# Kernel optimization log

Hardware: AMD Instinct MI355X
Metric: run time of the kernel (lower is better)

## Reference

```python
import jax, jax.numpy as jnp
import numpy as np

C = 64        # channel_n
HID = 128     # hidden_size
HEADS = 4
HD = 16       # head_dim = embed_dim // heads, embed_dim overwritten to channel_n
INNER = HEADS * HD  # 64
MLP = 64
H = W = 64    # img_size
B = 8
STEPS = 6
IN_CH = 1     # input_channels
SCALE = HD ** -0.5


def conv3x3_reflect(x, w, b):
    # x: [B,C,H,W], w: [O,I,3,3] -- reflect padding like nn.Conv2d(padding_mode='reflect')
    xp = jnp.pad(x, ((0, 0), (0, 0), (1, 1), (1, 1)), mode='reflect')
    y = jax.lax.conv_general_dilated(xp, w, (1, 1), 'VALID',
                                     dimension_numbers=('NCHW', 'OIHW', 'NCHW'))
    return y + b[None, :, None, None]


def layernorm(x, w, b, axes):
    mu = jnp.mean(x, axis=axes, keepdims=True)
    var = jnp.var(x, axis=axes, keepdims=True)
    return (x - mu) * jax.lax.rsqrt(var + 1e-5) * w + b


def localize(t, h, w):
    # t: [B,heads,n,d] -> [B,heads,n,9,d]; zero-padded 3x3 neighbourhoods
    # (equivalent to grouped conv with 9 unit-impulse filters, padding='same')
    b, nh, n, d = t.shape
    g = t.reshape(b, nh, h, w, d)
    gp = jnp.pad(g, ((0, 0), (0, 0), (1, 1), (1, 1), (0, 0)))
    nb = jnp.stack([gp[:, :, i:i + h, j:j + w, :]
                    for i in range(3) for j in range(3)], axis=4)
    return nb.reshape(b, nh, n, 9, d)


def attn_block(t, ln_w, ln_b, qkv_w, out_w, out_b):
    y = layernorm(t, ln_w, ln_b, -1)
    qkv = y @ qkv_w.T                              # [B,n,3*inner]
    q, k, v = jnp.split(qkv, 3, axis=-1)
    to_heads = lambda z: z.reshape(z.shape[0], z.shape[1], HEADS, HD).transpose(0, 2, 1, 3)
    q, k, v = to_heads(q), to_heads(k), to_heads(v)   # [B,h,n,d]
    kl = localize(k, H, W)                          # [B,h,n,9,d]
    vl = localize(v, H, W)
    dots = jnp.einsum('bhnd,bhnkd->bhnk', q, kl) * SCALE
    a = jax.nn.softmax(dots, axis=-1)               # [B,h,n,9]
    o = jnp.einsum('bhnk,bhnkd->bhnd', a, vl)
    o = o.transpose(0, 2, 1, 3).reshape(t.shape[0], t.shape[1], INNER)
    return o @ out_w.T + out_b


def ff_block(t, ln_w, ln_b, w1, b1, w2, b2):
    y = layernorm(t, ln_w, ln_b, -1)
    y = jax.nn.gelu(y @ w1.T + b1, approximate=False)
    return y @ w2.T + b2


def setup_inputs() -> dict:
    key = jax.random.key(0)
    ks = jax.random.split(key, 20)
    s = 0.02
    inp = {
        'x': jax.random.normal(ks[0], (B, H, W, C), jnp.float32),
        'masks': jax.random.bernoulli(ks[1], 0.5, (STEPS, B, H, W, 1)),
        'p0_w': jax.random.normal(ks[2], (C, C, 3, 3)) * s,
        'p0_b': jnp.zeros((C,)),
        'p1_w': jax.random.normal(ks[3], (C, C, 3, 3)) * s,
        'p1_b': jnp.zeros((C,)),
        'fc0_w': jax.random.normal(ks[4], (HID, 3 * C)) * s,
        'fc0_b': jnp.zeros((HID,)),
        'fc1_w': jax.random.normal(ks[5], (C, HID)) * s,  # zero-init in torch; random here for a non-trivial test
        'norm0_w': jnp.ones((H, W, HID)),
        'norm0_b': jnp.zeros((H, W, HID)),
        'ln1_w': jnp.ones((C,)),
        'ln1_b': jnp.zeros((C,)),
        'qkv_w': jax.random.normal(ks[6], (3 * INNER, C)) * s,
        'out_w': jax.random.normal(ks[7], (C, INNER)) * s,
        'out_b': jnp.zeros((C,)),
        'ln2_w': jnp.ones((C,)),
        'ln2_b': jnp.zeros((C,)),
        'ff1_w': jax.random.normal(ks[8], (MLP, C)) * s,
        'ff1_b': jnp.zeros((MLP,)),
        'ff2_w': jax.random.normal(ks[9], (C, MLP)) * s,
        'ff2_b': jnp.zeros((C,)),
        'steps': STEPS,
    }
    return inp


def reference(x, masks, p0_w, p0_b, p1_w, p1_b, fc0_w, fc0_b, fc1_w,
              norm0_w, norm0_b, ln1_w, ln1_b, qkv_w, out_w, out_b,
              ln2_w, ln2_b, ff1_w, ff1_b, ff2_w, ff2_b, steps):
    def step(xc, mask):
        # ---- NCA perception + update (BackboneNCA.perceive + fc0/relu/norm/fc1) ----
        xt = xc.transpose(0, 3, 1, 2)                      # [B,C,H,W]
        y1 = conv3x3_reflect(xt, p0_w, p0_b)
        y2 = conv3x3_reflect(xt, p1_w, p1_b)
        p = jnp.concatenate([xt, y1, y2], 1).transpose(0, 2, 3, 1)  # [B,H,W,3C]
        hd = jax.nn.relu(p @ fc0_w.T + fc0_b)              # [B,H,W,HID]
        hd = layernorm(hd, norm0_w, norm0_b, (-3, -2, -1))  # norm0 over [H,W,HID]
        dx = hd @ fc1_w.T                                   # [B,H,W,C]
        dx = dx * mask.astype(xc.dtype)                     # stochastic fire
        xn = xc + dx
        # ---- ViT block with localized (3x3 windowed) attention ----
        t = xn.reshape(B, H * W, C)
        t = t + attn_block(t, ln1_w, ln1_b, qkv_w, out_w, out_b)
        t = t + ff_block(t, ln2_w, ln2_b, ff1_w, ff1_b, ff2_w, ff2_b)
        xn = t.reshape(B, H, W, C)
        # keep input channels unchanged
        xn = jnp.concatenate([xc[..., :IN_CH], xn[..., IN_CH:]], axis=-1)
        return xn, None

    out, _ = jax.lax.scan(step, x, masks)
    return out
```

## Files before the change

### kernel.cpp

```cpp
#include <hip/hip_runtime.h>
#include <hip/hip_bf16.h>

typedef __hip_bfloat16 bf16;
typedef __attribute__((ext_vector_type(8))) short bf16x8;
typedef __attribute__((ext_vector_type(4))) float f32x4;

#define NSTEP 6

static __device__ __forceinline__ float b2f(bf16 v) { return __bfloat162float(v); }

static __device__ __forceinline__ float ldp(const void* p, int i, int md) {
    return md ? ((const float*)p)[i] : b2f(((const bf16*)p)[i]);
}
static __device__ __forceinline__ float finz(float v) {
    return (v == v && v * 0.0f == 0.0f) ? v : 0.0f;
}
static __device__ __forceinline__ unsigned short f2bfu(float v) {
    bf16 h = __float2bfloat16(v);
    return *(unsigned short*)&h;
}

static __device__ __forceinline__ void ld_bf8(const bf16* p, float* f) {
    union { uint4 u; unsigned short s[8]; } r;
    r.u = *(const uint4*)p;
#pragma unroll
    for (int j = 0; j < 8; ++j) f[j] = __uint_as_float(((unsigned)r.s[j]) << 16);
}
static __device__ __forceinline__ void ldp8(const void* p, int i, int md, float* f) {
    if (md) {
        const float* fp = (const float*)p + i;
        float4 a = *(const float4*)fp, b = *(const float4*)(fp + 4);
        f[0]=a.x; f[1]=a.y; f[2]=a.z; f[3]=a.w; f[4]=b.x; f[5]=b.y; f[6]=b.z; f[7]=b.w;
    } else {
        ld_bf8((const bf16*)p + i, f);
    }
}
static __device__ __forceinline__ uint4 pk_bf8(const float* f) {
    union { uint4 u; unsigned short s[8]; } r;
#pragma unroll
    for (int j = 0; j < 8; ++j) r.s[j] = f2bfu(f[j]);
    return r.u;
}


__global__ void k_detect(const uint4* __restrict__ m4,
                         const uint4* __restrict__ x4,
                         int* __restrict__ flags, float* __restrict__ accv) {
    __shared__ int s3f, sup, slo, sf32;
    int t = threadIdx.x;
    if (t == 0) { s3f = 0; sup = 0; slo = 0; sf32 = 0; }
    if (t < 96) accv[t] = 0.f;
    __syncthreads();
    int l3f = 0, lup = 0, llo = 0, lf = 0;
    for (int i = t; i < 3072; i += 256) {
        uint4 v = m4[i];
        const unsigned* d = (const unsigned*)&v;
#pragma unroll
        for (int j = 0; j < 4; ++j) {
            unsigned w = d[j];
            unsigned x3f = w ^ 0x3F3F3F3Fu;
            if ((x3f - 0x01010101u) & ~x3f & 0x80808080u) l3f = 1;
            if (w & 0xFFFFFF00u) lup = 1;
            if (w & 0x0000FFFFu) llo = 1;
        }
    }
    for (int i = t; i < 4096; i += 256) {
        uint4 v = x4[i];
        const unsigned* d = (const unsigned*)&v;
#pragma unroll
        for (int j = 0; j < 4; ++j) {
            unsigned bb = (d[j] >> 8) & 0x7Fu;
            if (bb > 0x48u) lf = 1;
        }
    }
    if (l3f) atomicOr(&s3f, 1);
    if (lup) atomicOr(&sup, 1);
    if (llo) atomicOr(&slo, 1);
    if (lf)  atomicOr(&sf32, 1);
    __syncthreads();
    if (t == 0) {
        int mode;
        if (!s3f && !sup) mode = 0;
        else if (!s3f)    mode = 1;
        else if (slo)     mode = 2;
        else              mode = 3;
        flags[0] = mode;
        flags[1] = sf32;
    }
}


template <int MD>
static __device__ __forceinline__ void cast_body(
    const void* __restrict__ x, float* __restrict__ xout, int i) {
    float f[8];
    ldp8(x, i * 8, MD, f);
#pragma unroll
    for (int j = 0; j < 8; ++j) f[j] = finz(f[j]);
    *(float4*)&xout[i * 8]     = make_float4(f[0], f[1], f[2], f[3]);
    *(float4*)&xout[i * 8 + 4] = make_float4(f[4], f[5], f[6], f[7]);
}

template <int MD>
static __device__ __forceinline__ void cwfold_body(
    const void* __restrict__ p0w, const void* __restrict__ p1w,
    const void* __restrict__ p0b, const void* __restrict__ p1b,
    const void* __restrict__ fc0w, const void* __restrict__ fc0b,
    short* __restrict__ cw, float* __restrict__ hbias,
    float* __restrict__ sfc0, int o, int t) {
    if (t < 192) sfc0[t] = ldp(fc0w, o * 192 + t, MD);
    __syncthreads();
    int u0 = t, u1 = t + 256, u2 = t + 512;
    bool has2 = (u2 < 576);
    float a0 = (u0 % 9 == 4) ? sfc0[u0 / 9] : 0.f;
    float a1 = (u1 % 9 == 4) ? sfc0[u1 / 9] : 0.f;
    float a2 = (has2 && u2 % 9 == 4) ? sfc0[u2 / 9] : 0.f;
#pragma unroll 8
    for (int c = 0; c < 64; ++c) {
        float f0 = sfc0[64 + c];
        float f1 = sfc0[128 + c];
        int base = c * 576;
        a0 = fmaf(ldp(p0w, base + u0, MD), f0, a0);
        a0 = fmaf(ldp(p1w, base + u0, MD), f1, a0);
        a1 = fmaf(ldp(p0w, base + u1, MD), f0, a1);
        a1 = fmaf(ldp(p1w, base + u1, MD), f1, a1);
        if (has2) {
            a2 = fmaf(ldp(p0w, base + u2, MD), f0, a2);
            a2 = fmaf(ldp(p1w, base + u2, MD), f1, a2);
        }
    }
    cw[o * 576 + (u0 % 9) * 64 + u0 / 9] = (short)f2bfu(a0);
    cw[o * 576 + (u1 % 9) * 64 + u1 / 9] = (short)f2bfu(a1);
    if (has2) cw[o * 576 + (u2 % 9) * 64 + u2 / 9] = (short)f2bfu(a2);
    if (t < 64) {
        int c = t;
        float s = ldp(p0b, c, MD) * sfc0[64 + c]
                + ldp(p1b, c, MD) * sfc0[128 + c];
#pragma unroll
        for (int off = 32; off > 0; off >>= 1) s += __shfl_down(s, off, 64);
        if (c == 0) hbias[o] = ldp(fc0b, o, MD) + s;
    }
}

template <int MD>
static __device__ __forceinline__ void lnfold_body(
    const void* __restrict__ fc1w, const void* __restrict__ n0w,
    const void* __restrict__ n0b, float* __restrict__ wsum,
    float* __restrict__ bconst, int pos, int c) {
    float ws = 0.f, bs = 0.f;
#pragma unroll 8
    for (int j8 = 0; j8 < 128; j8 += 8) {
        float wv[8], bv[8], fv[8];
        ldp8(n0w, pos * 128 + j8, MD, wv);
        ldp8(n0b, pos * 128 + j8, MD, bv);
        ldp8(fc1w, c * 128 + j8, MD, fv);
#pragma unroll
        for (int jj = 0; jj < 8; ++jj) {
            float f = __uint_as_float(((unsigned)f2bfu(fv[jj])) << 16);
            ws = fmaf(wv[jj], f, ws);
            bs = fmaf(bv[jj], f, bs);
        }
    }
    wsum[pos * 64 + c]   = ws;
    bconst[pos * 64 + c] = bs;
}

__global__ void k_prep_w(const void* __restrict__ p0w, const void* __restrict__ p1w,
                         const void* __restrict__ p0b, const void* __restrict__ p1b,
                         const void* __restrict__ fc0w, const void* __restrict__ fc0b,
                         const void* __restrict__ fc1w, const void* __restrict__ qkvw,
                         const void* __restrict__ outw, const void* __restrict__ ff1w,
                         const void* __restrict__ ff2w,
                         short* __restrict__ cw, short* __restrict__ packs,
                         float* __restrict__ hbias,
                         const void* __restrict__ n0w, const void* __restrict__ n0b,
                         float* __restrict__ wsum, float* __restrict__ bconst,
                         const int* __restrict__ mflags) {
    __shared__ float sfc0[192];
    int md = mflags[1];
    int t = threadIdx.x;
    int bk = blockIdx.x;
    if (bk < 128) {
        int j = bk * 256 + t;
        float v;
        if      (j < 8192)  v = ldp(fc1w, j, md);
        else if (j < 20480) v = ldp(qkvw, j - 8192, md);
        else if (j < 24576) v = ldp(outw, j - 20480, md);
        else if (j < 28672) v = ldp(ff1w, j - 24576, md);
        else                v = ldp(ff2w, j - 28672, md);
        packs[j] = (short)f2bfu(v);
    } else if (bk < 256) {
        int o = bk - 128;
        if (md) cwfold_body<1>(p0w, p1w, p0b, p1b, fc0w, fc0b, cw, hbias, sfc0, o, t);
        else    cwfold_body<0>(p0w, p1w, p0b, p1b, fc0w, fc0b, cw, hbias, sfc0, o, t);
    } else {
        int fbk = bk - 256;
        int c = t & 63, pl = t >> 6;
        int pos = fbk * 4 + pl;
        if (md) lnfold_body<1>(fc1w, n0w, n0b, wsum, bconst, pos, c);
        else    lnfold_body<0>(fc1w, n0w, n0b, wsum, bconst, pos, c);
    }
}

__global__ void k_prep_cast(const void* __restrict__ x, float* __restrict__ xout,
                            const int* __restrict__ mflags) {
    int md = mflags[1];
    int i = blockIdx.x * 256 + threadIdx.x;
    if (md) cast_body<1>(x, xout, i);
    else    cast_body<0>(x, xout, i);
}


__global__ __launch_bounds__(512) void k_perceive(
    const float* __restrict__ xin, const short* __restrict__ cw,
    const short* __restrict__ fc1s, const float* __restrict__ hbias,
    const void* __restrict__ n0w, const int* __restrict__ mflags,
    float* __restrict__ t1, float* __restrict__ accv, int step)
{
    __shared__ __align__(16) short xpad_s[3 * 66 * 72];
    __shared__ __align__(16) short hd_s[64 * 136];
    __shared__ float red[32];
    int md = mflags[1];
    int bh = blockIdx.x;
    int b = bh >> 6, h = bh & 63;
    int t = threadIdx.x;

    for (int e = t; e < 1536; e += 512) {
        int c8 = e & 7, w = (e >> 3) & 63, r = e >> 9;
        int hr = h - 1 + r; hr = hr < 0 ? -hr : (hr > 63 ? 126 - hr : hr);
        const float* src = xin + ((((b << 6) + hr) << 6) | w) * 64 + c8 * 8;
        float f[8];
        float4 v0 = *(const float4*)src, v1 = *(const float4*)(src + 4);
        f[0]=v0.x; f[1]=v0.y; f[2]=v0.z; f[3]=v0.w; f[4]=v1.x; f[5]=v1.y; f[6]=v1.z; f[7]=v1.w;
        *(uint4*)&xpad_s[((r * 66) + w + 1) * 72 + c8 * 8] = pk_bf8(f);
    }
    if (t < 48) {
        int c8 = t & 7, side = (t >> 3) & 1, r = t >> 4;
        int hr = h - 1 + r; hr = hr < 0 ? -hr : (hr > 63 ? 126 - hr : hr);
        int wsrc = side ? 62 : 1, wp = side ? 65 : 0;
        const float* src = xin + ((((b << 6) + hr) << 6) | wsrc) * 64 + c8 * 8;
        float f[8];
        float4 v0 = *(const float4*)src, v1 = *(const float4*)(src + 4);
        f[0]=v0.x; f[1]=v0.y; f[2]=v0.z; f[3]=v0.w; f[4]=v1.x; f[5]=v1.y; f[6]=v1.z; f[7]=v1.w;
        *(uint4*)&xpad_s[((r * 66) + wp) * 72 + c8 * 8] = pk_bf8(f);
    }
    __syncthreads();

    int og  = __builtin_amdgcn_readfirstlane(t >> 6);
    int l   = t & 63, nl = l & 15, q = l >> 4;
    int mt0 = (og & 1) * 2;
    int nt0 = (og >> 1) * 2;
    int o0  = nt0 * 16 + nl, o1 = o0 + 16;

    f32x4 acc[2][2];
#pragma unroll
    for (int i = 0; i < 2; ++i)
#pragma unroll
        for (int j = 0; j < 2; ++j) acc[i][j] = (f32x4){0.f, 0.f, 0.f, 0.f};

    for (int kt = 0; kt < 18; ++kt) {
        int kk = kt >> 1, c0 = (kt & 1) << 5;
        int r = kk / 3, cxi = kk - r * 3;
        bf16x8 b0 = *(const bf16x8*)(cw + o0 * 576 + kt * 32 + q * 8);
        bf16x8 b1 = *(const bf16x8*)(cw + o1 * 576 + kt * 32 + q * 8);
        bf16x8 a0 = *(const bf16x8*)&xpad_s[((r * 66) + mt0 * 16 + nl + cxi) * 72 + c0 + q * 8];
        bf16x8 a1 = *(const bf16x8*)&xpad_s[((r * 66) + mt0 * 16 + 16 + nl + cxi) * 72 + c0 + q * 8];
        acc[0][0] = __builtin_amdgcn_mfma_f32_16x16x32_bf16(a0, b0, acc[0][0], 0, 0, 0);
        acc[0][1] = __builtin_amdgcn_mfma_f32_16x16x32_bf16(a0, b1, acc[0][1], 0, 0, 0);
        acc[1][0] = __builtin_amdgcn_mfma_f32_16x16x32_bf16(a1, b0, acc[1][0], 0, 0, 0);
        acc[1][1] = __builtin_amdgcn_mfma_f32_16x16x32_bf16(a1, b1, acc[1][1], 0, 0, 0);
    }

    float lsum = 0.f, lsq = 0.f;
    {
        float hb0 = hbias[o0], hb1 = hbias[o1];
#pragma unroll
        for (int i = 0; i < 2; ++i)
#pragma unroll
            for (int j = 0; j < 2; ++j) {
                int oo = j ? o1 : o0;
                float bb = j ? hb1 : hb0;
#pragma unroll
                for (int r2 = 0; r2 < 4; ++r2) {
                    int m = (mt0 + i) * 16 + q * 4 + r2;
                    float v = fmaxf(acc[i][j][r2] + bb, 0.f);
                    unsigned short hu = f2bfu(v);
                    hd_s[m * 136 + oo] = (short)hu;
                    float vr = __uint_as_float(((unsigned)hu) << 16);
                    lsum += vr; lsq += vr * vr;
                }
            }
    }
#pragma unroll
    for (int off = 32; off > 0; off >>= 1) {
        lsum += __shfl_down(lsum, off, 64);
        lsq  += __shfl_down(lsq,  off, 64);
    }
    if (l == 0) { red[og] = lsum; red[16 + og] = lsq; }
    __syncthreads();
    if (t == 0) {
        float a = 0.f, s2 = 0.f;
#pragma unroll
        for (int w = 0; w < 8; ++w) { a += red[w]; s2 += red[16 + w]; }
        atomicAdd(&accv[step * 16 + b * 2],     a);
        atomicAdd(&accv[step * 16 + b * 2 + 1], s2);
    }

    for (int e = t; e < 1024; e += 512) {
        int pos = e >> 4, j8 = (e & 15) * 8;
        float hv[8], wv[8];
        ld_bf8((const bf16*)&hd_s[pos * 136 + j8], hv);
        ldp8(n0w, (h * 64 + pos) * 128 + j8, md, wv);
#pragma unroll
        for (int j = 0; j < 8; ++j) hv[j] *= wv[j];
        *(uint4*)&hd_s[pos * 136 + j8] = pk_bf8(hv);
    }
    __syncthreads();

    {
        int mt = og & 3, nh = og >> 2;
        int to0 = nh * 32 + nl, to1 = to0 + 16;
        f32x4 a0 = (f32x4){0.f,0.f,0.f,0.f}, a1 = (f32x4){0.f,0.f,0.f,0.f};
#pragma unroll
        for (int kt = 0; kt < 4; ++kt) {
            bf16x8 av = *(const bf16x8*)&hd_s[(mt * 16 + nl) * 136 + kt * 32 + q * 8];
            bf16x8 b0 = *(const bf16x8*)(fc1s + to0 * 128 + kt * 32 + q * 8);
            bf16x8 b1 = *(const bf16x8*)(fc1s + to1 * 128 + kt * 32 + q * 8);
            a0 = __builtin_amdgcn_mfma_f32_16x16x32_bf16(av, b0, a0, 0, 0, 0);
            a1 = __builtin_amdgcn_mfma_f32_16x16x32_bf16(av, b1, a1, 0, 0, 0);
        }
#pragma unroll
        for (int r2 = 0; r2 < 4; ++r2) {
            int m = mt * 16 + q * 4 + r2;
            t1[((bh << 6) + m) * 64 + to0] = a0[r2];
            t1[((bh << 6) + m) * 64 + to1] = a1[r2];
        }
    }
}

__global__ __launch_bounds__(512) void k_upd(
    const float* __restrict__ xin, float* __restrict__ xnew,
    const float* __restrict__ t1, const float* __restrict__ wsum,
    const float* __restrict__ bconst, const void* __restrict__ mraw,
    const short* __restrict__ qkvs, const void* __restrict__ ln1w,
    const void* __restrict__ ln1b, const int* __restrict__ mflags,
    const float* __restrict__ accv, bf16* __restrict__ qkv, int step)
{
    __shared__ __align__(16) short ys[64 * 72];
    __shared__ __align__(16) short qo[64 * 200];
    int md = mflags[1];
    int bh = blockIdx.x;
    int b = bh >> 6, h = bh & 63;
    int t = threadIdx.x;
    const float invN = 1.f / 524288.f;
    float mean = accv[step * 16 + b * 2] * invN;
    float var  = accv[step * 16 + b * 2 + 1] * invN - mean * mean;
    float rstd = rsqrtf(fmaxf(var, 0.f) + 1e-5f);
    float mrs  = mean * rstd;

    int tok = t >> 3, j8 = (t & 7) * 8;
    int idx = ((bh << 6) + tok) * 64 + j8;
    int ppos = (h * 64 + tok) * 64 + j8;
    {
        float4 x0 = *(const float4*)&xin[idx], x1 = *(const float4*)&xin[idx + 4];
        float xv[8] = {x0.x, x0.y, x0.z, x0.w, x1.x, x1.y, x1.z, x1.w};
        float4 a0 = *(const float4*)&t1[idx], a1 = *(const float4*)&t1[idx + 4];
        float tv[8] = {a0.x, a0.y, a0.z, a0.w, a1.x, a1.y, a1.z, a1.w};
        float4 w0 = *(const float4*)&wsum[ppos], w1 = *(const float4*)&wsum[ppos + 4];
        float wv[8] = {w0.x, w0.y, w0.z, w0.w, w1.x, w1.y, w1.z, w1.w};
        float4 b0 = *(const float4*)&bconst[ppos], b1 = *(const float4*)&bconst[ppos + 4];
        float bc[8] = {b0.x, b0.y, b0.z, b0.w, b1.x, b1.y, b1.z, b1.w};

        int mmode = mflags[0];
        int midx = ((step * 8 + b) * 64 + h) * 64 + tok;
        int mk;
        if (mmode == 0)      mk = ((const int*)mraw)[midx] != 0;
        else if (mmode == 1) mk = ((const unsigned char*)mraw)[midx] != 0;
        else if (mmode == 2) mk = ((const unsigned short*)mraw)[midx] != 0;
        else                 mk = ((const float*)mraw)[midx] != 0.0f;

        float vloc[8];
        float ls = 0.f, lq = 0.f;
#pragma unroll
        for (int ci = 0; ci < 8; ++ci) {
            float dx = rstd * tv[ci] - mrs * wv[ci] + bc[ci];
            vloc[ci] = finz(mk ? (xv[ci] + dx) : xv[ci]);
            ls += vloc[ci]; lq += vloc[ci] * vloc[ci];
        }
        *(float4*)&xnew[idx]     = make_float4(vloc[0], vloc[1], vloc[2], vloc[3]);
        *(float4*)&xnew[idx + 4] = make_float4(vloc[4], vloc[5], vloc[6], vloc[7]);
#pragma unroll
        for (int off = 1; off < 8; off <<= 1) {
            ls += __shfl_xor(ls, off, 64);
            lq += __shfl_xor(lq, off, 64);
        }
        float mu = ls * (1.f / 64.f);
        float vr = lq * (1.f / 64.f) - mu * mu;
        float rs = rsqrtf(fmaxf(vr, 0.f) + 1e-5f);
        float lw[8], lb[8];
        ldp8(ln1w, j8, md, lw);
        ldp8(ln1b, j8, md, lb);
        float yv[8];
#pragma unroll
        for (int ci = 0; ci < 8; ++ci)
            yv[ci] = (vloc[ci] - mu) * rs * lw[ci] + lb[ci];
        *(uint4*)&ys[tok * 72 + j8] = pk_bf8(yv);
    }
    __syncthreads();

    int og = __builtin_amdgcn_readfirstlane(t >> 6);
    int l = t & 63, nl = l & 15, q = l >> 4;
    {
        int mt = og & 3, nh2 = og >> 2;
        f32x4 qa[6];
#pragma unroll
        for (int n = 0; n < 6; ++n) qa[n] = (f32x4){0.f, 0.f, 0.f, 0.f};
#pragma unroll
        for (int kt = 0; kt < 2; ++kt) {
            bf16x8 av = *(const bf16x8*)&ys[(mt * 16 + nl) * 72 + kt * 32 + q * 8];
#pragma unroll
            for (int n = 0; n < 6; ++n) {
                bf16x8 bv = *(const bf16x8*)(qkvs + (((nh2 * 6 + n) * 16) + nl) * 64 + kt * 32 + q * 8);
                qa[n] = __builtin_amdgcn_mfma_f32_16x16x32_bf16(av, bv, qa[n], 0, 0, 0);
            }
        }
#pragma unroll
        for (int n = 0; n < 6; ++n)
#pragma unroll
            for (int r2 = 0; r2 < 4; ++r2) {
                int m = mt * 16 + q * 4 + r2;
                qo[m * 200 + (nh2 * 6 + n) * 16 + nl] = (short)f2bfu(qa[n][r2]);
            }
    }
    __syncthreads();

    for (int e = t; e < 1536; e += 512) {
        int p2 = e / 24, c8 = e - p2 * 24;
        *(uint4*)(qkv + ((bh << 6) + p2) * 192 + c8 * 8) =
            *(const uint4*)&qo[p2 * 200 + c8 * 8];
    }
}

__global__ __launch_bounds__(512) void k_attn_ff(
    const bf16* __restrict__ qkv, const float* __restrict__ xold,
    float* __restrict__ xnew, const short* __restrict__ outs,
    const short* __restrict__ ff1s, const short* __restrict__ ff2s,
    const void* __restrict__ outb, const void* __restrict__ ln2w,
    const void* __restrict__ ln2b, const void* __restrict__ ff1b,
    const void* __restrict__ ff2b, const int* __restrict__ mflags,
    void* __restrict__ dout, int write_out)
{
    __shared__ __align__(16) char smraw[66240];
    short* Ks = (short*)smraw;
    short* Vs = (short*)(smraw + 28512);
    short* Ao = (short*)(smraw + 57024);
    float* ts = (float*)smraw;
    short* ys = (short*)(smraw + 16640);
    short* hs = (short*)(smraw + 25856);

    int md = mflags[1];
    int bh = blockIdx.x;
    int b = bh >> 6, h = bh & 63;
    int t = threadIdx.x;
    int tok = t >> 3, j8 = (t & 7) * 8;
    int idx = ((bh << 6) + tok) * 64 + j8;

    float xn8[8];
    {
        float4 x0 = *(const float4*)&xnew[idx], x1 = *(const float4*)&xnew[idx + 4];
        xn8[0]=x0.x; xn8[1]=x0.y; xn8[2]=x0.z; xn8[3]=x0.w;
        xn8[4]=x1.x; xn8[5]=x1.y; xn8[6]=x1.z; xn8[7]=x1.w;
    }
    float c0 = (j8 == 0) ? xold[idx] : 0.f;

    if (t < 96) {
        int kind = (t >= 48) ? 1 : 0, u = t - kind * 48;
        int r = u >> 4, side = (u >> 3) & 1, c8 = u & 7;
        short* dst = kind ? Vs : Ks;
        uint4 z = {0, 0, 0, 0};
        *(uint4*)&dst[((r * 66) + (side ? 65 : 0)) * 72 + c8 * 8] = z;
    }
    for (int e = t; e < 3072; e += 512) {
        int kind = (e >= 1536) ? 1 : 0, u = e - kind * 1536;
        int c8 = u & 7, w = (u >> 3) & 63, r = u >> 9;
        int hr = h - 1 + r;
        uint4 v = {0, 0, 0, 0};
        if (hr >= 0 && hr <= 63)
            v = *(const uint4*)(qkv + ((b * 64 + hr) * 64 + w) * 192 + 64 + kind * 64 + c8 * 8);
        short* dst = kind ? Vs : Ks;
        *(uint4*)&dst[((r * 66) + w + 1) * 72 + c8 * 8] = v;
    }
    __syncthreads();

    int head = __builtin_amdgcn_readfirstlane(t >> 6) & 3;
    int pos  = t & 63;
    bool act = t < 256;
    if (act) {
        float qv[16];
        const bf16* qr = qkv + (((b * 64 + h) * 64) + pos) * 192 + head * 16;
        ld_bf8(qr, qv); ld_bf8(qr + 8, qv + 8);

        float a9[9];
#pragma unroll
        for (int r = 0; r < 3; ++r)
#pragma unroll
            for (int cxi = 0; cxi < 3; ++cxi) {
                const short* kp = &Ks[((r * 66) + pos + cxi) * 72 + head * 16];
                float kf[16];
                ld_bf8((const bf16*)kp, kf);
                ld_bf8((const bf16*)(kp + 8), kf + 8);
                float dot = 0.f;
#pragma unroll
                for (int d = 0; d < 16; ++d) dot = fmaf(qv[d], kf[d], dot);
                a9[r * 3 + cxi] = dot * 0.25f;
            }
        float mx = a9[0];
#pragma unroll
        for (int k = 1; k < 9; ++k) mx = fmaxf(mx, a9[k]);
        float ssum = 0.f;
#pragma unroll
        for (int k = 0; k < 9; ++k) { a9[k] = __expf(a9[k] - mx); ssum += a9[k]; }
        float inv = 1.f / ssum;
#pragma unroll
        for (int k = 0; k < 9; ++k) a9[k] *= inv;

        float o[16];
#pragma unroll
        for (int d = 0; d < 16; ++d) o[d] = 0.f;
#pragma unroll
        for (int r = 0; r < 3; ++r)
#pragma unroll
            for (int cxi = 0; cxi < 3; ++cxi) {
                const short* vp = &Vs[((r * 66) + pos + cxi) * 72 + head * 16];
                float vf[16];
                ld_bf8((const bf16*)vp, vf);
                ld_bf8((const bf16*)(vp + 8), vf + 8);
                float w = a9[r * 3 + cxi];
#pragma unroll
                for (int d = 0; d < 16; ++d) o[d] = fmaf(w, vf[d], o[d]);
            }
        *(uint4*)&Ao[pos * 72 + head * 16]     = pk_bf8(o);
        *(uint4*)&Ao[pos * 72 + head * 16 + 8] = pk_bf8(o + 8);
    }
    __syncthreads();

    int og = __builtin_amdgcn_readfirstlane(t >> 6);
    int l = t & 63, nl = l & 15, qd = l >> 4;
    int mt = og & 3;
    int nt0 = (og >> 2) * 2;
    int o0 = nt0 * 16 + nl, o1 = o0 + 16;

    {
        f32x4 pa[2];
        pa[0] = (f32x4){0.f,0.f,0.f,0.f}; pa[1] = (f32x4){0.f,0.f,0.f,0.f};
#pragma unroll
        for (int kt = 0; kt < 2; ++kt) {
            bf16x8 av = *(const bf16x8*)&Ao[(mt * 16 + nl) * 72 + kt * 32 + qd * 8];
            bf16x8 b0 = *(const bf16x8*)(outs + o0 * 64 + kt * 32 + qd * 8);
            bf16x8 b1 = *(const bf16x8*)(outs + o1 * 64 + kt * 32 + qd * 8);
            pa[0] = __builtin_amdgcn_mfma_f32_16x16x32_bf16(av, b0, pa[0], 0, 0, 0);
            pa[1] = __builtin_amdgcn_mfma_f32_16x16x32_bf16(av, b1, pa[1], 0, 0, 0);
        }
        float ob0 = ldp(outb, o0, md), ob1 = ldp(outb, o1, md);
#pragma unroll
        for (int j = 0; j < 2; ++j)
#pragma unroll
            for (int r2 = 0; r2 < 4; ++r2) {
                int m = mt * 16 + qd * 4 + r2;
                ts[m * 65 + (j ? o1 : o0)] = pa[j][r2] + (j ? ob1 : ob0);
            }
    }
    __syncthreads();

    {
        float v[8];
        float ls = 0.f, lq = 0.f;
#pragma unroll
        for (int ci = 0; ci < 8; ++ci) {
            v[ci] = ts[tok * 65 + j8 + ci] + xn8[ci];
            ts[tok * 65 + j8 + ci] = v[ci];
            ls += v[ci]; lq += v[ci] * v[ci];
        }
#pragma unroll
        for (int off = 1; off < 8; off <<= 1) {
            ls += __shfl_xor(ls, off, 64);
            lq += __shfl_xor(lq, off, 64);
        }
        float mu = ls * (1.f / 64.f);
        float vr = lq * (1.f / 64.f) - mu * mu;
        float rs = rsqrtf(fmaxf(vr, 0.f) + 1e-5f);
        float wv[8], bv[8];
        ldp8(ln2w, j8, md, wv);
        ldp8(ln2b, j8, md, bv);
        float yv[8];
#pragma unroll
        for (int ci = 0; ci < 8; ++ci) yv[ci] = (v[ci] - mu) * rs * wv[ci] + bv[ci];
        *(uint4*)&ys[tok * 72 + j8] = pk_bf8(yv);
    }
    __syncthreads();

    {
        f32x4 ma[2];
        ma[0] = (f32x4){0.f,0.f,0.f,0.f}; ma[1] = (f32x4){0.f,0.f,0.f,0.f};
#pragma unroll
        for (int kt = 0; kt < 2; ++kt) {
            bf16x8 av = *(const bf16x8*)&ys[(mt * 16 + nl) * 72 + kt * 32 + qd * 8];
            bf16x8 b0 = *(const bf16x8*)(ff1s + o0 * 64 + kt * 32 + qd * 8);
            bf16x8 b1 = *(const bf16x8*)(ff1s + o1 * 64 + kt * 32 + qd * 8);
            ma[0] = __builtin_amdgcn_mfma_f32_16x16x32_bf16(av, b0, ma[0], 0, 0, 0);
            ma[1] = __builtin_amdgcn_mfma_f32_16x16x32_bf16(av, b1, ma[1], 0, 0, 0);
        }
        float f1b0 = ldp(ff1b, o0, md), f1b1 = ldp(ff1b, o1, md);
#pragma unroll
        for (int j = 0; j < 2; ++j)
#pragma unroll
            for (int r2 = 0; r2 < 4; ++r2) {
                int m = mt * 16 + qd * 4 + r2;
                float v = ma[j][r2] + (j ? f1b1 : f1b0);
                float g = 0.5f * v * (1.f + erff(v * 0.70710678118654752f));
                hs[m * 72 + (j ? o1 : o0)] = (short)f2bfu(g);
            }
    }
    __syncthreads();

    {
        f32x4 fa[2];
        fa[0] = (f32x4){0.f,0.f,0.f,0.f}; fa[1] = (f32x4){0.f,0.f,0.f,0.f};
#pragma unroll
        for (int kt = 0; kt < 2; ++kt) {
            bf16x8 av = *(const bf16x8*)&hs[(mt * 16 + nl) * 72 + kt * 32 + qd * 8];
            bf16x8 b0 = *(const bf16x8*)(ff2s + o0 * 64 + kt * 32 + qd * 8);
            bf16x8 b1 = *(const bf16x8*)(ff2s + o1 * 64 + kt * 32 + qd * 8);
            fa[0] = __builtin_amdgcn_mfma_f32_16x16x32_bf16(av, b0, fa[0], 0, 0, 0);
            fa[1] = __builtin_amdgcn_mfma_f32_16x16x32_bf16(av, b1, fa[1], 0, 0, 0);
        }
        float f2b0 = ldp(ff2b, o0, md), f2b1 = ldp(ff2b, o1, md);
#pragma unroll
        for (int j = 0; j < 2; ++j)
#pragma unroll
            for (int r2 = 0; r2 < 4; ++r2) {
                int m = mt * 16 + qd * 4 + r2;
                int oo = j ? o1 : o0;
                ts[m * 65 + oo] += fa[j][r2] + (j ? f2b1 : f2b0);
            }
    }
    __syncthreads();

    {
        float fv[8];
#pragma unroll
        for (int ci = 0; ci < 8; ++ci) {
            float v = ts[tok * 65 + j8 + ci];
            if (j8 == 0 && ci == 0) v = c0;
            fv[ci] = finz(v);
        }
        *(float4*)&xnew[idx]     = make_float4(fv[0], fv[1], fv[2], fv[3]);
        *(float4*)&xnew[idx + 4] = make_float4(fv[4], fv[5], fv[6], fv[7]);
        if (write_out) {
            if (md) {
                *(float4*)&((float*)dout)[idx]     = make_float4(fv[0], fv[1], fv[2], fv[3]);
                *(float4*)&((float*)dout)[idx + 4] = make_float4(fv[4], fv[5], fv[6], fv[7]);
            } else {
                *(uint4*)&((bf16*)dout)[idx] = pk_bf8(fv);
            }
        }
    }
}


extern "C" void kernel_launch(void* const* d_in, const int* in_sizes, int n_in,
                              void* d_out, int out_size, void* d_ws, size_t ws_size,
                              hipStream_t stream) {
    (void)in_sizes; (void)n_in; (void)out_size; (void)ws_size;
    const void* x     = d_in[0];
    const void* masks = d_in[1];
    const void* p0w   = d_in[2];
    const void* p0b   = d_in[3];
    const void* p1w   = d_in[4];
    const void* p1b   = d_in[5];
    const void* fc0w  = d_in[6];
    const void* fc0b  = d_in[7];
    const void* fc1w  = d_in[8];
    const void* n0w   = d_in[9];
    const void* n0b   = d_in[10];
    const void* ln1w  = d_in[11];
    const void* ln1b  = d_in[12];
    const void* qkvw  = d_in[13];
    const void* outw  = d_in[14];
    const void* outb  = d_in[15];
    const void* ln2w  = d_in[16];
    const void* ln2b  = d_in[17];
    const void* ff1w  = d_in[18];
    const void* ff1b  = d_in[19];
    const void* ff2w  = d_in[20];
    const void* ff2b  = d_in[21];

    char* wsb = (char*)d_ws;
    float* xst0   = (float*)(wsb + 0);
    float* xst1   = (float*)(wsb + 8388608);
    float* t1buf  = (float*)(wsb + 16777216);
    bf16*  qkvb   = (bf16*) (wsb + 25165824);
    short* cw     = (short*)(wsb + 37748736);
    short* packs  = (short*)(wsb + 37896192);
    float* hbias  = (float*)(wsb + 37961728);
    float* wsumb  = (float*)(wsb + 37962240);
    float* bconb  = (float*)(wsb + 39010816);
    float* accv   = (float*)(wsb + 40059392);
    int*   mflags = (int*)  (wsb + 40059776);

    short* fc1s = packs;
    short* qkvs = packs + 8192;
    short* outs = packs + 20480;
    short* ff1s = packs + 24576;
    short* ff2s = packs + 28672;

    k_detect<<<1, 256, 0, stream>>>((const uint4*)masks, (const uint4*)x, mflags, accv);
    k_prep_w<<<1280, 256, 0, stream>>>(p0w, p1w, p0b, p1b, fc0w, fc0b,
                                       fc1w, qkvw, outw, ff1w, ff2w,
                                       cw, packs, hbias, n0w, n0b, wsumb, bconb, mflags);
    k_prep_cast<<<1024, 256, 0, stream>>>(x, xst0, mflags);

    float* xbuf[2] = {xst0, xst1};
    for (int s = 0; s < NSTEP; ++s) {
        float* cur = xbuf[s & 1];
        float* nxt = xbuf[(s + 1) & 1];
        k_perceive<<<512, 512, 0, stream>>>(cur, cw, fc1s, hbias, n0w, mflags,
                                            t1buf, accv, s);
        k_upd<<<512, 512, 0, stream>>>(cur, nxt, t1buf, wsumb, bconb, masks,
                                       qkvs, ln1w, ln1b, mflags, accv, qkvb, s);
        k_attn_ff<<<512, 512, 0, stream>>>(qkvb, cur, nxt, outs, ff1s, ff2s,
                                           outb, ln2w, ln2b, ff1b, ff2b, mflags,
                                           d_out, (s == NSTEP - 1) ? 1 : 0);
    }
}
```

Baseline: 581.6 us.

## Fuse perceive and update kernels using an in-kernel per-batch grid barrier

```diff
diff --git a/kernel.cpp b/kernel.cpp
--- a/kernel.cpp
+++ b/kernel.cpp
@@ -45,11 +45,13 @@
 
 __global__ void k_detect(const uint4* __restrict__ m4,
                          const uint4* __restrict__ x4,
-                         int* __restrict__ flags, float* __restrict__ accv) {
+                         int* __restrict__ flags, float* __restrict__ accv,
+                         int* __restrict__ cnt) {
     __shared__ int s3f, sup, slo, sf32;
     int t = threadIdx.x;
     if (t == 0) { s3f = 0; sup = 0; slo = 0; sf32 = 0; }
     if (t < 96) accv[t] = 0.f;
+    if (t < 48) cnt[t] = 0;
     __syncthreads();
     int l3f = 0, lup = 0, llo = 0, lf = 0;
     for (int i = t; i < 3072; i += 256) {
@@ -211,19 +213,30 @@
 }
 
 
-__global__ __launch_bounds__(512) void k_perceive(
-    const float* __restrict__ xin, const short* __restrict__ cw,
-    const short* __restrict__ fc1s, const float* __restrict__ hbias,
-    const void* __restrict__ n0w, const int* __restrict__ mflags,
-    float* __restrict__ t1, float* __restrict__ accv, int step)
+__global__ __launch_bounds__(512, 4) void k_percupd(
+    const float* __restrict__ xin, float* __restrict__ xnew,
+    const short* __restrict__ cw, const short* __restrict__ fc1s,
+    const float* __restrict__ hbias, const void* __restrict__ n0w,
+    const float* __restrict__ wsum, const float* __restrict__ bconst,
+    const void* __restrict__ mraw, const short* __restrict__ qkvs,
+    const void* __restrict__ ln1w, const void* __restrict__ ln1b,
+    const int* __restrict__ mflags, float* __restrict__ accv,
+    int* __restrict__ cnt, bf16* __restrict__ qkv, int step)
 {
-    __shared__ __align__(16) short xpad_s[3 * 66 * 72];
-    __shared__ __align__(16) short hd_s[64 * 136];
-    __shared__ float red[32];
+    __shared__ __align__(16) char sm[63584];
+    short* xpad = (short*)sm;
+    short* hd_s = (short*)(sm + 28512);
+    float* t1l  = (float*)(sm + 45920);
+    float* red  = (float*)(sm + 63328);
+    short* ys   = (short*)sm;
+    short* qo   = (short*)(sm + 9216);
+
     int md = mflags[1];
     int bh = blockIdx.x;
     int b = bh >> 6, h = bh & 63;
     int t = threadIdx.x;
+    int og = __builtin_amdgcn_readfirstlane(t >> 6);
+    int l = t & 63, nl = l & 15, q = l >> 4;
 
     for (int e = t; e < 1536; e += 512) {
         int c8 = e & 7, w = (e >> 3) & 63, r = e >> 9;
@@ -232,7 +245,7 @@
         float f[8];
         float4 v0 = *(const float4*)src, v1 = *(const float4*)(src + 4);
         f[0]=v0.x; f[1]=v0.y; f[2]=v0.z; f[3]=v0.w; f[4]=v1.x; f[5]=v1.y; f[6]=v1.z; f[7]=v1.w;
-        *(uint4*)&xpad_s[((r * 66) + w + 1) * 72 + c8 * 8] = pk_bf8(f);
+        *(uint4*)&xpad[((r * 66) + w + 1) * 72 + c8 * 8] = pk_bf8(f);
     }
     if (t < 48) {
         int c8 = t & 7, side = (t >> 3) & 1, r = t >> 4;
@@ -242,68 +255,71 @@
         float f[8];
         float4 v0 = *(const float4*)src, v1 = *(const float4*)(src + 4);
         f[0]=v0.x; f[1]=v0.y; f[2]=v0.z; f[3]=v0.w; f[4]=v1.x; f[5]=v1.y; f[6]=v1.z; f[7]=v1.w;
-        *(uint4*)&xpad_s[((r * 66) + wp) * 72 + c8 * 8] = pk_bf8(f);
-    }
-    __syncthreads();
-
-    int og  = __builtin_amdgcn_readfirstlane(t >> 6);
-    int l   = t & 63, nl = l & 15, q = l >> 4;
-    int mt0 = (og & 1) * 2;
-    int nt0 = (og >> 1) * 2;
-    int o0  = nt0 * 16 + nl, o1 = o0 + 16;
-
-    f32x4 acc[2][2];
-#pragma unroll
-    for (int i = 0; i < 2; ++i)
-#pragma unroll
-        for (int j = 0; j < 2; ++j) acc[i][j] = (f32x4){0.f, 0.f, 0.f, 0.f};
-
-    for (int kt = 0; kt < 18; ++kt) {
-        int kk = kt >> 1, c0 = (kt & 1) << 5;
-        int r = kk / 3, cxi = kk - r * 3;
-        bf16x8 b0 = *(const bf16x8*)(cw + o0 * 576 + kt * 32 + q * 8);
-        bf16x8 b1 = *(const bf16x8*)(cw + o1 * 576 + kt * 32 + q * 8);
-        bf16x8 a0 = *(const bf16x8*)&xpad_s[((r * 66) + mt0 * 16 + nl + cxi) * 72 + c0 + q * 8];
-        bf16x8 a1 = *(const bf16x8*)&xpad_s[((r * 66) + mt0 * 16 + 16 + nl + cxi) * 72 + c0 + q * 8];
-        acc[0][0] = __builtin_amdgcn_mfma_f32_16x16x32_bf16(a0, b0, acc[0][0], 0, 0, 0);
-        acc[0][1] = __builtin_amdgcn_mfma_f32_16x16x32_bf16(a0, b1, acc[0][1], 0, 0, 0);
-        acc[1][0] = __builtin_amdgcn_mfma_f32_16x16x32_bf16(a1, b0, acc[1][0], 0, 0, 0);
-        acc[1][1] = __builtin_amdgcn_mfma_f32_16x16x32_bf16(a1, b1, acc[1][1], 0, 0, 0);
-    }
-
-    float lsum = 0.f, lsq = 0.f;
-    {
-        float hb0 = hbias[o0], hb1 = hbias[o1];
+        *(uint4*)&xpad[((r * 66) + wp) * 72 + c8 * 8] = pk_bf8(f);
+    }
+    __syncthreads();
+
+    {
+        int mt0 = (og & 1) * 2;
+        int nt0 = (og >> 1) * 2;
+        int o0  = nt0 * 16 + nl, o1 = o0 + 16;
+
+        f32x4 acc[2][2];
 #pragma unroll
         for (int i = 0; i < 2; ++i)
 #pragma unroll
-            for (int j = 0; j < 2; ++j) {
-                int oo = j ? o1 : o0;
-                float bb = j ? hb1 : hb0;
-#pragma unroll
-                for (int r2 = 0; r2 < 4; ++r2) {
-                    int m = (mt0 + i) * 16 + q * 4 + r2;
-                    float v = fmaxf(acc[i][j][r2] + bb, 0.f);
-                    unsigned short hu = f2bfu(v);
-                    hd_s[m * 136 + oo] = (short)hu;
-                    float vr = __uint_as_float(((unsigned)hu) << 16);
-                    lsum += vr; lsq += vr * vr;
+            for (int j = 0; j < 2; ++j) acc[i][j] = (f32x4){0.f, 0.f, 0.f, 0.f};
+
+        for (int kt = 0; kt < 18; ++kt) {
+            int kk = kt >> 1, c0 = (kt & 1) << 5;
+            int r = kk / 3, cxi = kk - r * 3;
+            bf16x8 b0 = *(const bf16x8*)(cw + o0 * 576 + kt * 32 + q * 8);
+            bf16x8 b1 = *(const bf16x8*)(cw + o1 * 576 + kt * 32 + q * 8);
+            bf16x8 a0 = *(const bf16x8*)&xpad[((r * 66) + mt0 * 16 + nl + cxi) * 72 + c0 + q * 8];
+            bf16x8 a1 = *(const bf16x8*)&xpad[((r * 66) + mt0 * 16 + 16 + nl + cxi) * 72 + c0 + q * 8];
+            acc[0][0] = __builtin_amdgcn_mfma_f32_16x16x32_bf16(a0, b0, acc[0][0], 0, 0, 0);
+            acc[0][1] = __builtin_amdgcn_mfma_f32_16x16x32_bf16(a0, b1, acc[0][1], 0, 0, 0);
+            acc[1][0] = __builtin_amdgcn_mfma_f32_16x16x32_bf16(a1, b0, acc[1][0], 0, 0, 0);
+            acc[1][1] = __builtin_amdgcn_mfma_f32_16x16x32_bf16(a1, b1, acc[1][1], 0, 0, 0);
+        }
+
+        float lsum = 0.f, lsq = 0.f;
+        {
+            float hb0 = hbias[o0], hb1 = hbias[o1];
+#pragma unroll
+            for (int i = 0; i < 2; ++i)
+#pragma unroll
+                for (int j = 0; j < 2; ++j) {
+                    int oo = j ? o1 : o0;
+                    float bb = j ? hb1 : hb0;
+#pragma unroll
+                    for (int r2 = 0; r2 < 4; ++r2) {
+                        int m = (mt0 + i) * 16 + q * 4 + r2;
+                        float v = fmaxf(acc[i][j][r2] + bb, 0.f);
+                        unsigned short hu = f2bfu(v);
+                        hd_s[m * 136 + oo] = (short)hu;
+                        float vr = __uint_as_float(((unsigned)hu) << 16);
+                        lsum += vr; lsq += vr * vr;
+                    }
                 }
-            }
-    }
-#pragma unroll
-    for (int off = 32; off > 0; off >>= 1) {
-        lsum += __shfl_down(lsum, off, 64);
-        lsq  += __shfl_down(lsq,  off, 64);
-    }
-    if (l == 0) { red[og] = lsum; red[16 + og] = lsq; }
-    __syncthreads();
+        }
+#pragma unroll
+        for (int off = 32; off > 0; off >>= 1) {
+            lsum += __shfl_down(lsum, off, 64);
+            lsq  += __shfl_down(lsq,  off, 64);
+        }
+        if (l == 0) { red[og] = lsum; red[16 + og] = lsq; }
+    }
+    __syncthreads();
+
     if (t == 0) {
         float a = 0.f, s2 = 0.f;
 #pragma unroll
         for (int w = 0; w < 8; ++w) { a += red[w]; s2 += red[16 + w]; }
         atomicAdd(&accv[step * 16 + b * 2],     a);
         atomicAdd(&accv[step * 16 + b * 2 + 1], s2);
+        __hip_atomic_fetch_add(&cnt[step * 8 + b], 1,
+                               __ATOMIC_RELEASE, __HIP_MEMORY_SCOPE_AGENT);
     }
 
     for (int e = t; e < 1024; e += 512) {
@@ -332,40 +348,39 @@
 #pragma unroll
         for (int r2 = 0; r2 < 4; ++r2) {
             int m = mt * 16 + q * 4 + r2;
-            t1[((bh << 6) + m) * 64 + to0] = a0[r2];
-            t1[((bh << 6) + m) * 64 + to1] = a1[r2];
-        }
-    }
-}
-
-__global__ __launch_bounds__(512) void k_upd(
-    const float* __restrict__ xin, float* __restrict__ xnew,
-    const float* __restrict__ t1, const float* __restrict__ wsum,
-    const float* __restrict__ bconst, const void* __restrict__ mraw,
-    const short* __restrict__ qkvs, const void* __restrict__ ln1w,
-    const void* __restrict__ ln1b, const int* __restrict__ mflags,
-    const float* __restrict__ accv, bf16* __restrict__ qkv, int step)
-{
-    __shared__ __align__(16) short ys[64 * 72];
-    __shared__ __align__(16) short qo[64 * 200];
-    int md = mflags[1];
-    int bh = blockIdx.x;
-    int b = bh >> 6, h = bh & 63;
-    int t = threadIdx.x;
-    const float invN = 1.f / 524288.f;
-    float mean = accv[step * 16 + b * 2] * invN;
-    float var  = accv[step * 16 + b * 2 + 1] * invN - mean * mean;
-    float rstd = rsqrtf(fmaxf(var, 0.f) + 1e-5f);
-    float mrs  = mean * rstd;
-
+            t1l[m * 68 + to0] = a0[r2];
+            t1l[m * 68 + to1] = a1[r2];
+        }
+    }
+
+    if (t == 0) {
+        while (__hip_atomic_load(&cnt[step * 8 + b],
+                                 __ATOMIC_ACQUIRE, __HIP_MEMORY_SCOPE_AGENT) < 64)
+            __builtin_amdgcn_s_sleep(4);
+        unsigned ua = __hip_atomic_load((const unsigned*)&accv[step * 16 + b * 2],
+                                        __ATOMIC_RELAXED, __HIP_MEMORY_SCOPE_AGENT);
+        unsigned us = __hip_atomic_load((const unsigned*)&accv[step * 16 + b * 2 + 1],
+                                        __ATOMIC_RELAXED, __HIP_MEMORY_SCOPE_AGENT);
+        const float invN = 1.f / 524288.f;
+        float mean = __uint_as_float(ua) * invN;
+        float var  = __uint_as_float(us) * invN - mean * mean;
+        float rstd = rsqrtf(fmaxf(var, 0.f) + 1e-5f);
+        red[0] = mean;
+        red[1] = rstd;
+    }
+    __syncthreads();
+
+    float mean = red[0], rstd = red[1];
+    float mrs = mean * rstd;
     int tok = t >> 3, j8 = (t & 7) * 8;
     int idx = ((bh << 6) + tok) * 64 + j8;
-    int ppos = (h * 64 + tok) * 64 + j8;
     {
         float4 x0 = *(const float4*)&xin[idx], x1 = *(const float4*)&xin[idx + 4];
         float xv[8] = {x0.x, x0.y, x0.z, x0.w, x1.x, x1.y, x1.z, x1.w};
-        float4 a0 = *(const float4*)&t1[idx], a1 = *(const float4*)&t1[idx + 4];
+        float4 a0 = *(const float4*)&t1l[tok * 68 + j8];
+        float4 a1 = *(const float4*)&t1l[tok * 68 + j8 + 4];
         float tv[8] = {a0.x, a0.y, a0.z, a0.w, a1.x, a1.y, a1.z, a1.w};
+        int ppos = (h * 64 + tok) * 64 + j8;
         float4 w0 = *(const float4*)&wsum[ppos], w1 = *(const float4*)&wsum[ppos + 4];
         float wv[8] = {w0.x, w0.y, w0.z, w0.w, w1.x, w1.y, w1.z, w1.w};
         float4 b0 = *(const float4*)&bconst[ppos], b1 = *(const float4*)&bconst[ppos + 4];
@@ -408,8 +423,6 @@
     }
     __syncthreads();
 
-    int og = __builtin_amdgcn_readfirstlane(t >> 6);
-    int l = t & 63, nl = l & 15, q = l >> 4;
     {
         int mt = og & 3, nh2 = og >> 2;
         f32x4 qa[6];
@@ -698,15 +711,15 @@
     char* wsb = (char*)d_ws;
     float* xst0   = (float*)(wsb + 0);
     float* xst1   = (float*)(wsb + 8388608);
-    float* t1buf  = (float*)(wsb + 16777216);
-    bf16*  qkvb   = (bf16*) (wsb + 25165824);
-    short* cw     = (short*)(wsb + 37748736);
-    short* packs  = (short*)(wsb + 37896192);
-    float* hbias  = (float*)(wsb + 37961728);
-    float* wsumb  = (float*)(wsb + 37962240);
-    float* bconb  = (float*)(wsb + 39010816);
-    float* accv   = (float*)(wsb + 40059392);
-    int*   mflags = (int*)  (wsb + 40059776);
+    bf16*  qkvb   = (bf16*) (wsb + 16777216);
+    short* cw     = (short*)(wsb + 29360128);
+    short* packs  = (short*)(wsb + 29507584);
+    float* hbias  = (float*)(wsb + 29573120);
+    float* wsumb  = (float*)(wsb + 29573632);
+    float* bconb  = (float*)(wsb + 30622208);
+    float* accv   = (float*)(wsb + 31670784);
+    int*   mflags = (int*)  (wsb + 31671168);
+    int*   cnt    = (int*)  (wsb + 31671232);
 
     short* fc1s = packs;
     short* qkvs = packs + 8192;
@@ -714,7 +727,8 @@
     short* ff1s = packs + 24576;
     short* ff2s = packs + 28672;
 
-    k_detect<<<1, 256, 0, stream>>>((const uint4*)masks, (const uint4*)x, mflags, accv);
+    k_detect<<<1, 256, 0, stream>>>((const uint4*)masks, (const uint4*)x,
+                                    mflags, accv, cnt);
     k_prep_w<<<1280, 256, 0, stream>>>(p0w, p1w, p0b, p1b, fc0w, fc0b,
                                        fc1w, qkvw, outw, ff1w, ff2w,
                                        cw, packs, hbias, n0w, n0b, wsumb, bconb, mflags);
@@ -724,10 +738,9 @@
     for (int s = 0; s < NSTEP; ++s) {
         float* cur = xbuf[s & 1];
         float* nxt = xbuf[(s + 1) & 1];
-        k_perceive<<<512, 512, 0, stream>>>(cur, cw, fc1s, hbias, n0w, mflags,
-                                            t1buf, accv, s);
-        k_upd<<<512, 512, 0, stream>>>(cur, nxt, t1buf, wsumb, bconb, masks,
-                                       qkvs, ln1w, ln1b, mflags, accv, qkvb, s);
+        k_percupd<<<512, 512, 0, stream>>>(cur, nxt, cw, fc1s, hbias, n0w,
+                                           wsumb, bconb, masks, qkvs, ln1w, ln1b,
+                                           mflags, accv, cnt, qkvb, s);
         k_attn_ff<<<512, 512, 0, stream>>>(qkvb, cur, nxt, outs, ff1s, ff2s,
                                            outb, ln2w, ln2b, ff1b, ff2b, mflags,
                                            d_out, (s == NSTEP - 1) ? 1 : 0);
```

Result: no change. 591.2 us (+1.7%).
